# Kernel optimization log

Measured on AMD Instinct MI355X. Metric: run time of the kernel, lower is better.

The kernel has to match this reference:

```python
import jax, jax.numpy as jnp
import numpy as np

N = 50000
E = 800000
FEAT = 128
HID = 128
HEADS = 8
HEAD_DIM = HID // HEADS  # 16
NEG_SLOPE = 0.2


def _gat_layer(x, W, a_src, a_dst, b, src, dst, num_nodes):
    # x: [N, Fin]; W: [Fin, H*C]; a_src/a_dst: [H, C]; b: [H*C]
    H, C = a_src.shape
    h = (x @ W).reshape(num_nodes, H, C)               # [N,H,C]
    alpha_s = jnp.einsum('nhc,hc->nh', h, a_src)       # [N,H]
    alpha_d = jnp.einsum('nhc,hc->nh', h, a_dst)       # [N,H]
    e = jax.nn.leaky_relu(alpha_s[src] + alpha_d[dst], NEG_SLOPE)  # [E,H]
    # segment softmax over destination nodes (every node has a self-loop)
    m = jax.ops.segment_max(e, dst, num_segments=num_nodes)
    e = jnp.exp(e - m[dst])
    s = jax.ops.segment_sum(e, dst, num_segments=num_nodes)
    alpha = e / (s[dst] + 1e-16)                       # [E,H]
    msg = alpha[:, :, None] * h[src]                   # [E,H,C]
    out = jax.ops.segment_sum(msg, dst, num_segments=num_nodes)
    return out.reshape(num_nodes, H * C) + b


def setup_inputs() -> dict:
    key = jax.random.key(0)
    ks = jax.random.split(key, 12)
    x = jax.random.normal(ks[0], (N, FEAT), dtype=jnp.float32)
    edge_index = jax.random.randint(ks[1], (2, E), 0, N, dtype=jnp.int32)
    glorot = lambda k, shape: jax.random.uniform(
        k, shape, jnp.float32,
        -jnp.sqrt(6.0 / (shape[-2] + shape[-1])),
        jnp.sqrt(6.0 / (shape[-2] + shape[-1])))
    W1 = glorot(ks[2], (FEAT, HID))
    a_src1 = glorot(ks[3], (HEADS, HEAD_DIM))
    a_dst1 = glorot(ks[4], (HEADS, HEAD_DIM))
    b1 = jnp.zeros((HID,), jnp.float32)
    W2 = glorot(ks[5], (HID, HID))
    a_src2 = glorot(ks[6], (HEADS, HEAD_DIM))
    a_dst2 = glorot(ks[7], (HEADS, HEAD_DIM))
    b2 = jnp.zeros((HID,), jnp.float32)
    return {"x": x, "edge_index": edge_index,
            "W1": W1, "a_src1": a_src1, "a_dst1": a_dst1, "b1": b1,
            "W2": W2, "a_src2": a_src2, "a_dst2": a_dst2, "b2": b2}


def reference(x, edge_index, W1, a_src1, a_dst1, b1, W2, a_src2, a_dst2, b2):
    # GATConv adds self-loops to the (dense_to_sparse-derived) edge list
    loops = jnp.arange(N, dtype=edge_index.dtype)
    src = jnp.concatenate([edge_index[0], loops])
    dst = jnp.concatenate([edge_index[1], loops])
    h = _gat_layer(x, W1, a_src1, a_dst1, b1, src, dst, N)
    h = jax.nn.elu(h)
    # dropout: inference mode (training=False) -> identity
    h = _gat_layer(h, W2, a_src2, a_dst2, b2, src, dst, N)
    return jax.nn.elu(h)
```

## Files before the change

kernel.cpp:

```cpp
#include <hip/hip_runtime.h>
#include <hip/hip_fp16.h>
#include <math.h>

#define DEGMAX 64
#define CHUNK  2048
#define CAPB   6144

typedef _Float16 half8 __attribute__((ext_vector_type(8)));
typedef float    f32x4 __attribute__((ext_vector_type(4)));

__global__ __launch_bounds__(256) void k_csr(
        const int* __restrict__ gcur, const unsigned* __restrict__ bstore,
        int N, int* __restrict__ cnt, int* __restrict__ offs,
        unsigned short* __restrict__ adj) {
    int b = blockIdx.x;
    int t = threadIdx.x;
    int n0 = b << 8;
    int nb = N - n0; if (nb > 256) nb = 256;
    int ecnt = gcur[b]; if (ecnt > CAPB) ecnt = CAPB;
    __shared__ int lcnt[256], lofs[256], wsum[4];
    __shared__ unsigned short stage[CAPB];
    const unsigned* bp = bstore + (size_t)b * CAPB;

    lcnt[t] = 0;
    __syncthreads();
    for (int i = t; i < ecnt; i += 256)
        atomicAdd(&lcnt[bp[i] >> 16], 1);
    __syncthreads();
    int mycnt = lcnt[t];
    int lane = t & 63, wv = t >> 6;
    int x = mycnt;
    #pragma unroll
    for (int d = 1; d < 64; d <<= 1) {
        int y = __shfl_up(x, d);
        if (lane >= d) x += y;
    }
    if (lane == 63) wsum[wv] = x;
    __syncthreads();
    int base = 0;
    for (int k = 0; k < wv; k++) base += wsum[k];
    int myofs = base + x - mycnt;
    lofs[t] = myofs;
    if (t < nb) {
        cnt[n0 + t]  = mycnt;
        offs[n0 + t] = b * CAPB + myofs;
    }
    __syncthreads();
    lcnt[t] = 0;
    __syncthreads();
    for (int i = t; i < ecnt; i += 256) {
        unsigned p = bp[i];
        int node = p >> 16;
        int r = atomicAdd(&lcnt[node], 1);
        stage[lofs[node] + r] = (unsigned short)(p & 0xffffu);
    }
    __syncthreads();
    for (int i = t; i < ecnt; i += 256)
        adj[(size_t)b * CAPB + i] = stage[i];
}

__global__ void k_wcast(const float* __restrict__ W1, const float* __restrict__ as1,
                        const float* __restrict__ ad1, __half* __restrict__ Wf1,
                        const float* __restrict__ W2, const float* __restrict__ as2,
                        const float* __restrict__ ad2, __half* __restrict__ Wf2,
                        int* __restrict__ gcur) {
    int t = threadIdx.x;
    if (blockIdx.x == 0) gcur[t] = 0;
    int id2 = blockIdx.x * 256 + t;
    if (id2 >= 4608) return;
    int layer = id2 >= 2304 ? 1 : 0;
    const float* W  = layer ? W2  : W1;
    const float* av_s = layer ? as2 : as1;
    const float* av_d = layer ? ad2 : ad1;
    __half* Wf = layer ? Wf2 : Wf1;
    int id = id2 - layer * 2304;
    int lane = id & 63;
    int ct = (id >> 6) % 9;
    int kc = id / 576;
    int q = lane >> 4, n = lane & 15;
    #pragma unroll
    for (int j = 0; j < 8; j++) {
        int k = kc * 32 + q * 8 + j;
        float val;
        if (ct < 8) {
            val = W[(size_t)k * 128 + ct * 16 + n];
        } else {
            int h = n & 7;
            const float* a = (n < 8) ? av_s : av_d;
            float s = 0.f;
            #pragma unroll
            for (int c = 0; c < 16; c++)
                s += W[(size_t)k * 128 + h * 16 + c] * a[h * 16 + c];
            val = s;
        }
        Wf[(size_t)id * 8 + j] = __float2half(val);
    }
}

__device__ inline float4 ld4f(const float* p) { return *(const float4*)p; }

template<typename InT>
__device__ __forceinline__ void gemm_body(
        const InT* __restrict__ X, const __half* __restrict__ Wfrag,
        __half* __restrict__ H16, float* __restrict__ as_out,
        float* __restrict__ ad_out, int M, int bid) {
    __shared__ __half xls[64][136];
    int t = threadIdx.x;
    int w = t >> 6, lane = t & 63;
    int q = lane >> 4, n = lane & 15;
    int row0 = bid * 64;

    half8 bfrag[4][2];
    #pragma unroll
    for (int kc = 0; kc < 4; kc++)
        #pragma unroll
        for (int c2 = 0; c2 < 2; c2++) {
            int ct = w * 2 + c2;
            uint4 u = *(const uint4*)(Wfrag + (((size_t)(kc * 9 + ct)) * 64 + lane) * 8);
            bfrag[kc][c2] = *(half8*)&u;
        }
    half8 bfa[4];
    if (w == 0) {
        #pragma unroll
        for (int kc = 0; kc < 4; kc++) {
            uint4 u = *(const uint4*)(Wfrag + (((size_t)(kc * 9 + 8)) * 64 + lane) * 8);
            bfa[kc] = *(half8*)&u;
        }
    }

    #pragma unroll
    for (int rep = 0; rep < 8; rep++) {
        int lin = rep * 1024 + t * 4;
        int r = lin >> 7, k = lin & 127;
        int gr = row0 + r;
        uint2 u;
        if constexpr (sizeof(InT) == 4) {
            float4 v = (gr < M) ? ld4f((const float*)&X[(size_t)gr * 128 + k])
                                : make_float4(0.f, 0.f, 0.f, 0.f);
            __half2 h0 = __floats2half2_rn(v.x, v.y);
            __half2 h1 = __floats2half2_rn(v.z, v.w);
            u = make_uint2(*(unsigned*)&h0, *(unsigned*)&h1);
        } else {
            u = (gr < M) ? *(const uint2*)&X[(size_t)gr * 128 + k] : make_uint2(0, 0);
        }
        *(uint2*)&xls[r][k] = u;
    }
    __syncthreads();

    f32x4 acc[4][2], acca[4];
    #pragma unroll
    for (int rt = 0; rt < 4; rt++) {
        acc[rt][0] = (f32x4){0.f, 0.f, 0.f, 0.f};
        acc[rt][1] = (f32x4){0.f, 0.f, 0.f, 0.f};
        acca[rt]   = (f32x4){0.f, 0.f, 0.f, 0.f};
    }

    #pragma unroll
    for (int kc = 0; kc < 4; kc++)
        #pragma unroll
        for (int rt = 0; rt < 4; rt++) {
            uint4 au = *(const uint4*)&xls[rt * 16 + n][kc * 32 + q * 8];
            half8 af = *(half8*)&au;
            acc[rt][0] = __builtin_amdgcn_mfma_f32_16x16x32_f16(af, bfrag[kc][0], acc[rt][0], 0, 0, 0);
            acc[rt][1] = __builtin_amdgcn_mfma_f32_16x16x32_f16(af, bfrag[kc][1], acc[rt][1], 0, 0, 0);
            if (w == 0)
                acca[rt] = __builtin_amdgcn_mfma_f32_16x16x32_f16(af, bfa[kc], acca[rt], 0, 0, 0);
        }

    #pragma unroll
    for (int c2 = 0; c2 < 2; c2++) {
        int h = w * 2 + c2;
        #pragma unroll
        for (int rt = 0; rt < 4; rt++)
            #pragma unroll
            for (int reg = 0; reg < 4; reg++) {
                int grow = row0 + rt * 16 + q * 4 + reg;
                if (grow < M)
                    H16[(size_t)grow * 128 + h * 16 + n] = __float2half(acc[rt][c2][reg]);
            }
    }
    if (w == 0) {
        float* aout = (n < 8) ? as_out : ad_out;
        int h = n & 7;
        #pragma unroll
        for (int rt = 0; rt < 4; rt++)
            #pragma unroll
            for (int reg = 0; reg < 4; reg++) {
                int grow = row0 + rt * 16 + q * 4 + reg;
                if (grow < M) aout[grow * 8 + h] = acca[rt][reg];
            }
    }
}

__global__ __launch_bounds__(256) void k_bin_gemm(
        const float* __restrict__ X, const __half* __restrict__ Wfrag,
        __half* __restrict__ H16, float* __restrict__ as_out,
        float* __restrict__ ad_out, int M, int Gg,
        const int* __restrict__ src, const int* __restrict__ dst, int E, int K,
        int* __restrict__ gcur, unsigned* __restrict__ bstore) {
    int bid = blockIdx.x;
    if (bid < Gg) {
        gemm_body<float>(X, Wfrag, H16, as_out, ad_out, M, bid);
        return;
    }
    __shared__ int lcnt[256];
    __shared__ int gbase[256];
    int t = threadIdx.x;
    if (t < K) lcnt[t] = 0;
    __syncthreads();
    int e0 = (bid - Gg) * CHUNK;
    unsigned pk[8]; short bk[8], rk[8];
    #pragma unroll
    for (int j = 0; j < 8; j++) {
        int e = e0 + t + j * 256;
        bool v = e < E;
        int s = v ? src[e] : 0;
        int d = v ? dst[e] : 0;
        int b = d >> 8;
        pk[j] = ((unsigned)(d & 255) << 16) | (unsigned)s;
        bk[j] = (short)b;
        rk[j] = v ? (short)atomicAdd(&lcnt[b], 1) : (short)-1;
    }
    __syncthreads();
    if (t < K) gbase[t] = lcnt[t] ? atomicAdd(&gcur[t], lcnt[t]) : 0;
    __syncthreads();
    #pragma unroll
    for (int j = 0; j < 8; j++) {
        if (rk[j] >= 0) {
            int b = bk[j];
            int pos = gbase[b] + rk[j];
            if (pos < CAPB) bstore[(size_t)b * CAPB + pos] = pk[j];
        }
    }
}

__global__ __launch_bounds__(256) void k_gemm_mfma_h(
        const __half* __restrict__ X, const __half* __restrict__ Wfrag,
        __half* __restrict__ H16, float* __restrict__ as_out,
        float* __restrict__ ad_out, int M) {
    gemm_body<__half>(X, Wfrag, H16, as_out, ad_out, M, blockIdx.x);
}

#define LOADB(ii, LG, HR)                                                     \
    {                                                                         \
        int e_ = (ii) + (lane >> 3);                                          \
        int se_ = __shfl(sv, (e_ < deg) ? e_ : 0);                            \
        LG = as_[(size_t)se_ * 8 + (lane & 7)];                               \
        _Pragma("unroll")                                                     \
        for (int j_ = 0; j_ < 8; j_++) {                                      \
            int idx_ = (ii) + j_; if (idx_ >= deg) idx_ = deg - 1;            \
            int sj_ = __shfl(sv, idx_);                                       \
            HR[j_] = *(const unsigned*)&H[(size_t)sj_ * 128 + lane * 2];      \
        }                                                                     \
    }

#define COMPB(ii, LG, HR)                                                     \
    {                                                                         \
        float v_ = LG + adv;                                                  \
        v_ = v_ > 0.f ? v_ : 0.2f * v_;                                       \
        float wgt_ = ((ii) + (lane >> 3) < deg) ? __expf(v_) : 0.f;           \
        _Pragma("unroll")                                                     \
        for (int j_ = 0; j_ < 8; j_++) {                                      \
            float wj_ = __shfl(wgt_, j_ * 8 + hd);                            \
            float2 hv_ = __half22float2(*(__half2*)&HR[j_]);                  \
            ssum += wj_; ax += wj_ * hv_.x; ay += wj_ * hv_.y;                \
        }                                                                     \
    }

template<typename OutT>
__global__ __launch_bounds__(256) void k_aggregate(
        const __half* __restrict__ H, const float* __restrict__ as_,
        const float* __restrict__ ad_, const int* __restrict__ cnt,
        const int* __restrict__ offs, const unsigned short* __restrict__ adj,
        const float* __restrict__ bias, OutT* __restrict__ out, int N) {
    int wave = (int)((blockIdx.x * blockDim.x + threadIdx.x) >> 6);
    int lane = threadIdx.x & 63;
    if (wave >= N) return;
    int n = wave;
    int hd = lane >> 3;
    int deg = cnt[n]; if (deg > DEGMAX) deg = DEGMAX;
    int row = offs[n];
    int sv = (lane < deg) ? (int)adj[row + lane] : n;
    float adv = ad_[n * 8 + (lane & 7)];

    float vs = as_[n * 8 + hd] + ad_[n * 8 + hd];
    vs = vs > 0.f ? vs : 0.2f * vs;
    float wsf = __expf(vs);
    unsigned hrs = *(const unsigned*)&H[(size_t)n * 128 + lane * 2];
    float2 hvs = __half22float2(*(__half2*)&hrs);
    float ssum = wsf, ax = wsf * hvs.x, ay = wsf * hvs.y;

    float lg0, lg1, lg2, lg3;
    unsigned hr0[8], hr1[8], hr2[8], hr3[8];
    if (deg > 0)  LOADB(0,  lg0, hr0);
    if (deg > 8)  LOADB(8,  lg1, hr1);
    if (deg > 16) LOADB(16, lg2, hr2);
    if (deg > 24) LOADB(24, lg3, hr3);
    if (deg > 0)  COMPB(0,  lg0, hr0);
    if (deg > 8)  COMPB(8,  lg1, hr1);
    if (deg > 16) COMPB(16, lg2, hr2);
    if (deg > 24) COMPB(24, lg3, hr3);
    for (int i = 32; i < deg; i += 8) {
        float lgt; unsigned hrt[8];
        LOADB(i, lgt, hrt);
        COMPB(i, lgt, hrt);
    }

    float inv = 1.f / (ssum + 1e-16f);
    float ox = ax * inv + bias[lane * 2];
    float oy = ay * inv + bias[lane * 2 + 1];
    ox = ox > 0.f ? ox : __expf(ox) - 1.f;
    oy = oy > 0.f ? oy : __expf(oy) - 1.f;
    if constexpr (sizeof(OutT) == 2) {
        __half2 hv = __floats2half2_rn(ox, oy);
        *(__half2*)&out[(size_t)n * 128 + lane * 2] = hv;
    } else {
        *(float2*)&out[(size_t)n * 128 + lane * 2] = make_float2(ox, oy);
    }
}

static inline char* bump(char*& w, size_t bytes) {
    char* p = w;
    w += (bytes + 255) & ~(size_t)255;
    return p;
}

extern "C" void kernel_launch(void* const* d_in, const int* in_sizes, int n_in,
                              void* d_out, int out_size, void* d_ws, size_t ws_size,
                              hipStream_t stream) {
    const float* x   = (const float*)d_in[0];
    const int*   ei  = (const int*)d_in[1];
    const float* W1  = (const float*)d_in[2];
    const float* as1 = (const float*)d_in[3];
    const float* ad1 = (const float*)d_in[4];
    const float* b1  = (const float*)d_in[5];
    const float* W2  = (const float*)d_in[6];
    const float* as2 = (const float*)d_in[7];
    const float* ad2 = (const float*)d_in[8];
    const float* b2  = (const float*)d_in[9];
    float* out = (float*)d_out;

    int N = in_sizes[0] / 128;
    int E = in_sizes[1] / 2;
    const int* srcs = ei;
    const int* dsts = ei + E;
    int K = (N + 255) >> 8;
    int Gg = (N + 63) / 64;
    int Bb = (E + CHUNK - 1) / CHUNK;

    char* w = (char*)d_ws;
    int*            cnt   = (int*)           bump(w, (size_t)N * sizeof(int));
    int*            offs  = (int*)           bump(w, (size_t)N * sizeof(int));
    int*            gcur  = (int*)           bump(w, 256 * sizeof(int));
    unsigned*       bst   = (unsigned*)      bump(w, (size_t)256 * CAPB * sizeof(unsigned));
    unsigned short* adj   = (unsigned short*)bump(w, (size_t)256 * CAPB * sizeof(unsigned short));
    __half*         H16   = (__half*)        bump(w, (size_t)N * 128 * sizeof(__half));
    __half*         A16   = (__half*)        bump(w, (size_t)N * 128 * sizeof(__half));
    float*          asb   = (float*)         bump(w, (size_t)N * 8 * sizeof(float));
    float*          adb   = (float*)         bump(w, (size_t)N * 8 * sizeof(float));
    __half*         Wf1   = (__half*)        bump(w, 18432 * sizeof(__half));
    __half*         Wf2   = (__half*)        bump(w, 18432 * sizeof(__half));

    k_wcast<<<18, 256, 0, stream>>>(W1, as1, ad1, Wf1, W2, as2, ad2, Wf2, gcur);
    k_bin_gemm<<<Gg + Bb, 256, 0, stream>>>(x, Wf1, H16, asb, adb, N, Gg,
                                            srcs, dsts, E, K, gcur, bst);
    k_csr<<<K, 256, 0, stream>>>(gcur, bst, N, cnt, offs, adj);
    k_aggregate<__half><<<(N + 3) / 4, 256, 0, stream>>>(H16, asb, adb, cnt, offs, adj, b1, A16, N);
    k_gemm_mfma_h<<<Gg, 256, 0, stream>>>(A16, Wf2, H16, asb, adb, N);
    k_aggregate<float><<<(N + 3) / 4, 256, 0, stream>>>(H16, asb, adb, cnt, offs, adj, b2, out, N);
}
```

Baseline: 218.2 us.

## Split CSR build into half-bucket blocks and pad global bucket counters

Each 256-node destination bucket is now processed by two CSR blocks, each handling 128 nodes and writing to its own half of the bucket's adjacency region. This doubles the block count of the CSR stage, which previously had only about 196 blocks, and halves per-block shared staging. The global bucket cursors are also spaced 16 ints apart so atomics from the binning kernel hit separate cache lines. In exchange, each block scans the full bucket's edge list and drops edges beyond half capacity, which could truncate nodes in a skewed half-bucket.

After: 220.4 us. About the same (+1.0%).

```diff
diff --git a/kernel.cpp b/kernel.cpp
--- a/kernel.cpp
+++ b/kernel.cpp
@@ -5,6 +5,7 @@
 #define DEGMAX 64
 #define CHUNK  2048
 #define CAPB   6144
+#define HCAP   (CAPB / 2)
 
 typedef _Float16 half8 __attribute__((ext_vector_type(8)));
 typedef float    f32x4 __attribute__((ext_vector_type(4)));
@@ -13,21 +14,25 @@
         const int* __restrict__ gcur, const unsigned* __restrict__ bstore,
         int N, int* __restrict__ cnt, int* __restrict__ offs,
         unsigned short* __restrict__ adj) {
-    int b = blockIdx.x;
+    int blk = blockIdx.x;
+    int b = blk >> 1, hh = blk & 1;
+    int n0 = b * 256 + hh * 128;
+    int nb = N - n0; if (nb > 128) nb = 128; if (nb < 0) nb = 0;
+    int ecnt = gcur[b * 16]; if (ecnt > CAPB) ecnt = CAPB;
+    const unsigned* bp = bstore + (size_t)b * CAPB;
+    __shared__ int lcnt[128], lofs[128], wsum[2];
+    __shared__ unsigned short stage[HCAP];
     int t = threadIdx.x;
-    int n0 = b << 8;
-    int nb = N - n0; if (nb > 256) nb = 256;
-    int ecnt = gcur[b]; if (ecnt > CAPB) ecnt = CAPB;
-    __shared__ int lcnt[256], lofs[256], wsum[4];
-    __shared__ unsigned short stage[CAPB];
-    const unsigned* bp = bstore + (size_t)b * CAPB;
-
-    lcnt[t] = 0;
-    __syncthreads();
-    for (int i = t; i < ecnt; i += 256)
-        atomicAdd(&lcnt[bp[i] >> 16], 1);
-    __syncthreads();
-    int mycnt = lcnt[t];
+    int lo = hh * 128;
+
+    if (t < 128) lcnt[t] = 0;
+    __syncthreads();
+    for (int i = t; i < ecnt; i += 256) {
+        int node = bp[i] >> 16;
+        if ((node >> 7) == hh) atomicAdd(&lcnt[node - lo], 1);
+    }
+    __syncthreads();
+    int mycnt = (t < 128) ? lcnt[t] : 0;
     int lane = t & 63, wv = t >> 6;
     int x = mycnt;
     #pragma unroll
@@ -35,28 +40,34 @@
         int y = __shfl_up(x, d);
         if (lane >= d) x += y;
     }
-    if (lane == 63) wsum[wv] = x;
-    __syncthreads();
-    int base = 0;
-    for (int k = 0; k < wv; k++) base += wsum[k];
-    int myofs = base + x - mycnt;
-    lofs[t] = myofs;
+    if (lane == 63 && wv < 2) wsum[wv] = x;
+    __syncthreads();
+    int base0 = (wv == 1) ? wsum[0] : 0;
+    int myofs = base0 + x - mycnt;
+    if (t < 128) lofs[t] = myofs;
     if (t < nb) {
         cnt[n0 + t]  = mycnt;
-        offs[n0 + t] = b * CAPB + myofs;
-    }
-    __syncthreads();
-    lcnt[t] = 0;
+        offs[n0 + t] = b * CAPB + hh * HCAP + myofs;
+    }
+    __syncthreads();
+    if (t < 128) lcnt[t] = 0;
     __syncthreads();
     for (int i = t; i < ecnt; i += 256) {
         unsigned p = bp[i];
         int node = p >> 16;
-        int r = atomicAdd(&lcnt[node], 1);
-        stage[lofs[node] + r] = (unsigned short)(p & 0xffffu);
-    }
-    __syncthreads();
-    for (int i = t; i < ecnt; i += 256)
-        adj[(size_t)b * CAPB + i] = stage[i];
+        if ((node >> 7) == hh) {
+            int ln = node - lo;
+            int r = atomicAdd(&lcnt[ln], 1);
+            int pos = lofs[ln] + r;
+            if (pos < HCAP) stage[pos] = (unsigned short)(p & 0xffffu);
+        }
+    }
+    __syncthreads();
+    int total = wsum[0] + wsum[1];
+    if (total > HCAP) total = HCAP;
+    unsigned short* ap = adj + (size_t)b * CAPB + hh * HCAP;
+    for (int i = t; i < total; i += 256)
+        ap[i] = stage[i];
 }
 
 __global__ void k_wcast(const float* __restrict__ W1, const float* __restrict__ as1,
@@ -65,8 +76,8 @@
                         const float* __restrict__ ad2, __half* __restrict__ Wf2,
                         int* __restrict__ gcur) {
     int t = threadIdx.x;
-    if (blockIdx.x == 0) gcur[t] = 0;
     int id2 = blockIdx.x * 256 + t;
+    if (id2 < 4096) gcur[id2] = 0;
     if (id2 >= 4608) return;
     int layer = id2 >= 2304 ? 1 : 0;
     const float* W  = layer ? W2  : W1;
@@ -222,7 +233,7 @@
         rk[j] = v ? (short)atomicAdd(&lcnt[b], 1) : (short)-1;
     }
     __syncthreads();
-    if (t < K) gbase[t] = lcnt[t] ? atomicAdd(&gcur[t], lcnt[t]) : 0;
+    if (t < K) gbase[t] = lcnt[t] ? atomicAdd(&gcur[t * 16], lcnt[t]) : 0;
     __syncthreads();
     #pragma unroll
     for (int j = 0; j < 8; j++) {
@@ -351,7 +362,7 @@
     char* w = (char*)d_ws;
     int*            cnt   = (int*)           bump(w, (size_t)N * sizeof(int));
     int*            offs  = (int*)           bump(w, (size_t)N * sizeof(int));
-    int*            gcur  = (int*)           bump(w, 256 * sizeof(int));
+    int*            gcur  = (int*)           bump(w, 4096 * sizeof(int));
     unsigned*       bst   = (unsigned*)      bump(w, (size_t)256 * CAPB * sizeof(unsigned));
     unsigned short* adj   = (unsigned short*)bump(w, (size_t)256 * CAPB * sizeof(unsigned short));
     __half*         H16   = (__half*)        bump(w, (size_t)N * 128 * sizeof(__half));
@@ -364,7 +375,7 @@
     k_wcast<<<18, 256, 0, stream>>>(W1, as1, ad1, Wf1, W2, as2, ad2, Wf2, gcur);
     k_bin_gemm<<<Gg + Bb, 256, 0, stream>>>(x, Wf1, H16, asb, adb, N, Gg,
                                             srcs, dsts, E, K, gcur, bst);
-    k_csr<<<K, 256, 0, stream>>>(gcur, bst, N, cnt, offs, adj);
+    k_csr<<<2 * K, 256, 0, stream>>>(gcur, bst, N, cnt, offs, adj);
     k_aggregate<__half><<<(N + 3) / 4, 256, 0, stream>>>(H16, asb, adb, cnt, offs, adj, b1, A16, N);
     k_gemm_mfma_h<<<Gg, 256, 0, stream>>>(A16, Wf2, H16, asb, adb, N);
     k_aggregate<float><<<(N + 3) / 4, 256, 0, stream>>>(H16, asb, adb, cnt, offs, adj, b2, out, N);
```
